# Performance work log

Hardware: AMD Instinct MI355X
Metric: run time of the kernel (lower is better)

## Reference

```python
import jax, jax.numpy as jnp
import numpy as np
from functools import partial

B, L, V = 64, 512, 20000
P, M = 150, 6          # total patterns, max pattern length
NEG = -1e9             # semiring zero (log-space)
END_STATES = np.repeat(np.array([3, 4, 5]), 50)  # pattern_len-1 per pattern


@jax.custom_vjp
def ste_heaviside(x):
    return (x > 0).astype(x.dtype)

def _ste_fwd(x):
    return ste_heaviside(x), None

def _ste_bwd(_, g):
    return (g,)  # straight-through identity (matches torch code path)

ste_heaviside.defvjp(_ste_fwd, _ste_bwd)


def setup_inputs() -> dict:
    key = jax.random.key(0)
    ks = jax.random.split(key, 8)
    return {
        "docs": jax.random.randint(ks[0], (B, L), 0, V),
        "doc_lens": jax.random.randint(ks[1], (B,), 1, L),
        "local_embeddings": jax.random.normal(ks[2], (300, V), jnp.float32),
        "diags": jax.random.normal(ks[3], (P * M, 300), jnp.float32) * 0.05,
        "bias": jax.random.normal(ks[4], (P * M, 1), jnp.float32) * 0.05,
        "wildcards": jax.random.normal(ks[5], (P, M - 1), jnp.float32) * 0.05,
        "ln_gamma": jnp.ones((P,), jnp.float32),
        "ln_beta": jnp.zeros((P,), jnp.float32),
        "linear_w": jax.random.normal(ks[6], (2, P), jnp.float32) * 0.05,
        "linear_b": jnp.zeros((2,), jnp.float32),
    }


def reference(docs, doc_lens, local_embeddings, diags, bias, wildcards,
              ln_gamma, ln_beta, linear_w, linear_b):
    end_states = jnp.asarray(END_STATES)                  # [P]
    pat_idx = jnp.arange(P)

    # transition matrices over local vocab, mapped into log-space semiring
    tm_vocab = jax.nn.log_sigmoid((diags @ local_embeddings + bias).T)  # [V, P*M]
    tm = tm_vocab[docs].reshape(B, L, P, M)               # [B,L,P,M]

    # wildcard transitions: semiring.times(one=0, log_sigmoid(wildcards))
    wild = jax.nn.log_sigmoid(wildcards)                  # [P, M-1]

    restart = jnp.zeros((B, P, 1), tm.dtype)              # semiring one
    hid0 = jnp.full((B, P, M), NEG, tm.dtype).at[:, :, 0].set(0.0)
    scores0 = jnp.full((B, P), NEG, tm.dtype)             # semiring zero

    def step(carry, inputs):
        hid, sc = carry
        t, tm_t = inputs                                  # tm_t: [B,P,M]
        main = jnp.concatenate([restart, hid[:, :, :-1] + tm_t[:, :, :-1]], axis=2)
        wildp = jnp.concatenate([restart, hid[:, :, :-1] + wild[None]], axis=2)
        hid = jnp.maximum(main, wildp)                    # semiring plus
        esv = hid[:, pat_idx, end_states]                 # [B,P]
        active = (doc_lens > t)[:, None]
        sc = jnp.where(active, jnp.maximum(sc, esv), sc)
        return (hid, sc), None

    xs = (jnp.arange(L), jnp.moveaxis(tm, 1, 0))          # [L], [L,B,P,M]
    (_, scores), _ = jax.lax.scan(step, (hid0, scores0), xs)

    scores = jnp.exp(scores)                              # from_semiring_to_outer
    mu = scores.mean(axis=-1, keepdims=True)
    var = scores.var(axis=-1, keepdims=True)
    norm = (scores - mu) * jax.lax.rsqrt(var + 1e-5) * ln_gamma + ln_beta
    binar = ste_heaviside(norm)
    return binar @ linear_w.T + linear_b
```

## Files before the change

kernel.cpp:

```cpp
#include <hip/hip_runtime.h>
#include <hip/hip_bf16.h>
#include <hip/hip_fp16.h>
#include <math.h>

#define B_   64
#define L_   512
#define V_   20000
#define P_   150
#define M_   6
#define KDIM 300
#define NOUT 750
#define CWS  752
#define NEGF (-1.0e9f)

#define BM 128
#define BN 128
#define BK 16
#define LDP 132

#define KP 320
#define NIT 10
#define NVG 157
#define NJ  6
#define TILE_U4 1024
#define SA 1024.0f
#define SB 16384.0f
#define INV24 (5.9604644775390625e-8f)

#define TCHUNK 32
#define NCHUNK (L_ / TCHUNK)
#define WARM   5
#define CS_STRIDE 160
#define KVBUF 3

typedef _Float16 f16x8 __attribute__((ext_vector_type(8)));
typedef float f32x16 __attribute__((ext_vector_type(16)));

__device__ __forceinline__ float logsigf(float x) {
    return fminf(x, 0.f) - log1pf(expf(-fabsf(x)));
}

__device__ __forceinline__ float logsigf_fast(float x) {
    return fminf(x, 0.f) - __logf(1.f + __expf(-fabsf(x)));
}

__device__ __forceinline__ void gload_lds16(const void* gp, void* lp) {
    __builtin_amdgcn_global_load_lds(
        (const __attribute__((address_space(1))) unsigned int*)gp,
        (__attribute__((address_space(3))) unsigned int*)lp, 16, 0, 0);
}


__global__ __launch_bounds__(256) void p12_split(
    const float* __restrict__ emb, const float* __restrict__ diags,
    uint4* __restrict__ a_t, uint4* __restrict__ b_t)
{
    __shared__ float T[64][132];
    const int t   = threadIdx.x;
    const int bid = blockIdx.x;

    if (bid < NVG * 5) {
        const int gx = bid % NVG;
        const int ky = bid / NVG;
        const int v0 = gx * 128;
        const int k0 = ky * 64;

        #pragma unroll
        for (int pass = 0; pass < 8; ++pass) {
            int flat = pass * 256 + t;
            int krow = flat >> 5;
            int c4   = (flat & 31) * 4;
            int kg   = k0 + krow;
            int v    = v0 + c4;
            float4 f = {0.f, 0.f, 0.f, 0.f};
            if (kg < KDIM && v + 3 < V_)
                f = *(const float4*)(emb + (size_t)kg * V_ + v);
            *(float4*)&T[krow][c4] = f;
        }
        __syncthreads();

        const int vv = t >> 1;
        const int kh = (t & 1) * 32;
        const int it = ky * 2 + (kh >> 5);
        const int v  = v0 + vv;
        if (v < V_) {
            union { ushort u[8]; uint4 q; } H[4], Lo[4];
            #pragma unroll
            for (int i = 0; i < 32; ++i) {
                float x = T[kh + i][vv] * SA;
                __half h = __float2half_rn(x);
                float rem = x - __half2float(h);
                H[i >> 3].u[i & 7]  = __half_as_ushort(h);
                Lo[i >> 3].u[i & 7] = __half_as_ushort(__float2half_rn(rem));
            }
            uint4* tile = a_t + ((size_t)gx * NIT + it) * TILE_U4;
            #pragma unroll
            for (int c = 0; c < 4; ++c) {
                tile[      c * 128 + vv] = H[c].q;
                tile[512 + c * 128 + vv] = Lo[c].q;
            }
        }
    } else {
        const int bidx = bid - NVG * 5;
        const int it   = bidx % NIT;
        const int j    = bidx / NIT;
        const int row  = t >> 1;
        const int qh   = (t & 1) * 2;
        const int n    = j * 128 + row;
        const bool nok = (n < NOUT);
        const int pm   = nok ? ((n / 5) * 6 + (n % 5)) : 0;
        uint4* tile = b_t + (size_t)bidx * TILE_U4;
        #pragma unroll
        for (int qq = 0; qq < 2; ++qq) {
            int q = qh + qq;
            union { ushort u[8]; uint4 v; } H, Lo;
            #pragma unroll
            for (int e = 0; e < 8; ++e) {
                int k = it * 32 + q * 8 + e;
                float x = (nok && k < KDIM) ? diags[(size_t)pm * KDIM + k] * SB : 0.f;
                __half h = __float2half_rn(x);
                float rem = x - __half2float(h);
                H.u[e]  = __half_as_ushort(h);
                Lo.u[e] = __half_as_ushort(__float2half_rn(rem));
            }
            tile[      q * 128 + row] = H.v;
            tile[512 + q * 128 + row] = Lo.v;
        }
    }
}

__global__ __launch_bounds__(256, 2) void k1m_gemm(
    const uint4* __restrict__ a_t, const uint4* __restrict__ b_t,
    const float* __restrict__ bias, const float* __restrict__ wildc,
    float* __restrict__ cw)
{
    const int bid  = blockIdx.x;
    const int xcd  = bid & 7;
    const int slot = bid >> 3;
    const int g    = xcd + 8 * (slot / 6);
    const int j    = slot % 6;
    if (g >= NVG) return;

    __shared__ uint4 sm[2][2048];
    const int t    = threadIdx.x;
    const int lane = t & 63;
    const int w    = t >> 6;
    const int wr   = w >> 1, wc = w & 1;
    const int v0   = g * 128;
    const int n0   = j * 128;

    const uint4* gsec = (w < 2)
        ? a_t + (size_t)g * NIT * TILE_U4 + w * 512
        : b_t + (size_t)j * NIT * TILE_U4 + (w - 2) * 512;

    const int fk16 = lane >> 5;
    const int fm   = lane & 31;

    f32x16 acc[2][2];
    #pragma unroll
    for (int i = 0; i < 2; ++i)
        #pragma unroll
        for (int jj = 0; jj < 2; ++jj)
            #pragma unroll
            for (int r = 0; r < 16; ++r) acc[i][jj][r] = 0.f;

    {
        const uint4* gp = gsec + lane;
        #pragma unroll
        for (int i = 0; i < 8; ++i)
            gload_lds16(gp + i * 64, &sm[0][w * 512 + i * 64 + lane]);
    }

    int cur = 0;
    for (int it = 0; it < NIT; ++it) {
        __syncthreads();

        if (it + 1 < NIT) {
            const uint4* gp = gsec + (size_t)(it + 1) * TILE_U4 + lane;
            #pragma unroll
            for (int i = 0; i < 8; ++i)
                gload_lds16(gp + i * 64, &sm[cur ^ 1][w * 512 + i * 64 + lane]);
        }

        const uint4* smc = sm[cur];
        #pragma unroll
        for (int s = 0; s < 2; ++s) {
            f16x8 A1[2], A2[2], B1[2], B2[2];
            const int q = s * 2 + fk16;
            #pragma unroll
            for (int ri = 0; ri < 2; ++ri) {
                A1[ri] = *(const f16x8*)&smc[(0 * 4 + q) * 128 + wr * 64 + ri * 32 + fm];
                A2[ri] = *(const f16x8*)&smc[(1 * 4 + q) * 128 + wr * 64 + ri * 32 + fm];
            }
            #pragma unroll
            for (int cj = 0; cj < 2; ++cj) {
                B1[cj] = *(const f16x8*)&smc[(2 * 4 + q) * 128 + wc * 64 + cj * 32 + fm];
                B2[cj] = *(const f16x8*)&smc[(3 * 4 + q) * 128 + wc * 64 + cj * 32 + fm];
            }
            #pragma unroll
            for (int ri = 0; ri < 2; ++ri)
                #pragma unroll
                for (int cj = 0; cj < 2; ++cj) {
                    acc[ri][cj] = __builtin_amdgcn_mfma_f32_32x32x16_f16(A1[ri], B1[cj], acc[ri][cj], 0, 0, 0);
                    acc[ri][cj] = __builtin_amdgcn_mfma_f32_32x32x16_f16(A1[ri], B2[cj], acc[ri][cj], 0, 0, 0);
                    acc[ri][cj] = __builtin_amdgcn_mfma_f32_32x32x16_f16(A2[ri], B1[cj], acc[ri][cj], 0, 0, 0);
                }
        }
        cur ^= 1;
    }

    float biasv[2], lwv[2]; int ncol[2]; bool nok[2];
    #pragma unroll
    for (int cj = 0; cj < 2; ++cj) {
        int n = n0 + wc * 64 + cj * 32 + fm;
        ncol[cj] = n;
        nok[cj]  = (n < NOUT);
        int nc = nok[cj] ? n : 0;
        int pm = (nc / 5) * 6 + (nc % 5);
        biasv[cj] = bias[pm];
        lwv[cj]   = logsigf_fast(wildc[nc]);
    }
    #pragma unroll
    for (int ri = 0; ri < 2; ++ri) {
        int vbase = v0 + wr * 64 + ri * 32 + 4 * fk16;
        #pragma unroll
        for (int cj = 0; cj < 2; ++cj) {
            if (!nok[cj]) continue;
            #pragma unroll
            for (int r = 0; r < 16; ++r) {
                int v = vbase + (r & 3) + 8 * (r >> 2);
                if (v < V_) {
                    float val = acc[ri][cj][r] * INV24 + biasv[cj];
                    __builtin_nontemporal_store(
                        fmaxf(logsigf_fast(val), lwv[cj]),
                        &cw[(size_t)v * CWS + ncol[cj]]);
                }
            }
        }
    }
}


__global__ __launch_bounds__(256) void k1_gemm_cw(
    const float* __restrict__ emb,
    const float* __restrict__ diags,
    const float* __restrict__ bias,
    const float* __restrict__ wildc,
    float* __restrict__ cw)
{
    __shared__ float As[BK][LDP];
    __shared__ float Bs[BK][LDP];

    const int tid = threadIdx.x;
    const int v0 = blockIdx.x * BM;
    const int n0 = blockIdx.y * BN;
    const int tx = tid & 15;
    const int ty = tid >> 4;

    float acc[8][8];
    #pragma unroll
    for (int i = 0; i < 8; ++i)
        #pragma unroll
        for (int j = 0; j < 8; ++j) acc[i][j] = 0.f;

    const int a_k = tid >> 4;
    const int a_v = (tid & 15) * 8;
    const int b_n   = tid >> 1;
    const int b_kof = (tid & 1) * 8;

    int  brow;
    bool bval;
    {
        int n = n0 + b_n;
        bval = (n < NOUT);
        brow = bval ? ((n / 5) * 6 + (n % 5)) : 0;
    }

    for (int k0 = 0; k0 < KDIM; k0 += BK) {
        {
            float4 f0 = {0,0,0,0}, f1 = {0,0,0,0};
            int k = k0 + a_k;
            if (k < KDIM) {
                const float* src = emb + (size_t)k * V_ + v0 + a_v;
                if (v0 + a_v + 3 < V_) f0 = *(const float4*)src;
                if (v0 + a_v + 7 < V_) f1 = *(const float4*)(src + 4);
            }
            *(float4*)&As[a_k][a_v]     = f0;
            *(float4*)&As[a_k][a_v + 4] = f1;
        }
        {
            float4 f = {0,0,0,0}, g = {0,0,0,0};
            if (bval) {
                const float* src = diags + (size_t)brow * KDIM + k0 + b_kof;
                if (k0 + b_kof + 3 < KDIM) f = *(const float4*)src;
                if (k0 + b_kof + 7 < KDIM) g = *(const float4*)(src + 4);
            }
            Bs[b_kof + 0][b_n] = f.x;
            Bs[b_kof + 1][b_n] = f.y;
            Bs[b_kof + 2][b_n] = f.z;
            Bs[b_kof + 3][b_n] = f.w;
            Bs[b_kof + 4][b_n] = g.x;
            Bs[b_kof + 5][b_n] = g.y;
            Bs[b_kof + 6][b_n] = g.z;
            Bs[b_kof + 7][b_n] = g.w;
        }
        __syncthreads();
        #pragma unroll
        for (int k = 0; k < BK; ++k) {
            float4 a0 = *(const float4*)&As[k][tx * 4];
            float4 a1 = *(const float4*)&As[k][64 + tx * 4];
            float4 b0 = *(const float4*)&Bs[k][ty * 8];
            float4 b1 = *(const float4*)&Bs[k][ty * 8 + 4];
            float av[8] = {a0.x, a0.y, a0.z, a0.w, a1.x, a1.y, a1.z, a1.w};
            float bv[8] = {b0.x, b0.y, b0.z, b0.w, b1.x, b1.y, b1.z, b1.w};
            #pragma unroll
            for (int i = 0; i < 8; ++i)
                #pragma unroll
                for (int j = 0; j < 8; ++j)
                    acc[i][j] = fmaf(av[i], bv[j], acc[i][j]);
        }
        __syncthreads();
    }

    float biasv[8], lwv[8];
    #pragma unroll
    for (int j = 0; j < 8; ++j) {
        int n  = n0 + ty * 8 + j;
        int nc = (n < NOUT) ? n : 0;
        int pm = (nc / 5) * 6 + (nc % 5);
        biasv[j] = bias[pm];
        lwv[j]   = logsigf(wildc[nc]);
    }
    #pragma unroll
    for (int i = 0; i < 8; ++i) {
        int v = v0 + ((i < 4) ? (tx * 4 + i) : (64 + tx * 4 + (i - 4)));
        if (v >= V_) continue;
        float r[8];
        #pragma unroll
        for (int j = 0; j < 8; ++j)
            r[j] = fmaxf(logsigf(acc[i][j] + biasv[j]), lwv[j]);
        float* dst = cw + (size_t)v * CWS + n0 + ty * 8;
        if (n0 + ty * 8     < NOUT) *(float4*)dst       = make_float4(r[0], r[1], r[2], r[3]);
        if (n0 + ty * 8 + 4 < NOUT) *(float4*)(dst + 4) = make_float4(r[4], r[5], r[6], r[7]);
    }
}


__global__ __launch_bounds__(192) void k2_scan(
    const int* __restrict__ docs,
    const int* __restrict__ doc_lens,
    const float* __restrict__ cw,
    float* __restrict__ cs)
{
    const int ci = blockIdx.x;
    const int b  = blockIdx.y;
    const int t0 = ci * TCHUNK;
    const int ts = (t0 >= WARM) ? (t0 - WARM) : 0;
    const int dl = doc_lens[b];
    const int te = min(t0 + TCHUNK, dl);
    const int nt = te - ts;

    __shared__ int   toks[TCHUNK + WARM];
    __shared__ float rows[KVBUF][3][768];

    const int t    = threadIdx.x;
    const int lane = t & 63;
    const int w    = t >> 6;

    if (t < TCHUNK + WARM) {
        int tt = ts + t;
        toks[t] = docs[b * L_ + min(tt, L_ - 1)];
    }
    __syncthreads();

    const int p      = t;
    const int e      = (p < 50) ? 3 : (p < 100) ? 4 : 5;
    const int warm_n = t0 - ts;
    float h1 = NEGF, h2 = NEGF, h3 = NEGF, h4 = NEGF, h5 = NEGF, sc = NEGF;

    const int nrounds = (nt > 0) ? (nt + 2) / 3 : 0;

    for (int r0 = 0; r0 < 2; ++r0) {
        if (r0 >= nrounds) break;
        int idx = min(3 * r0 + w, nt - 1);
        const char* rowp = (const char*)(cw + (size_t)toks[idx] * CWS);
        char* lbase = (char*)&rows[r0][w][0];
        #pragma unroll
        for (int jj = 0; jj < 3; ++jj)
            gload_lds16(rowp + jj * 1024 + lane * 16,
                        lbase + jj * 1024 + lane * 16);
    }

    int bufc = 0;
    for (int r = 0; r < nrounds; ++r) {
        if (r + 1 < nrounds) {
            asm volatile("s_waitcnt vmcnt(3)" ::: "memory");
        } else {
            asm volatile("s_waitcnt vmcnt(0)" ::: "memory");
        }
        __builtin_amdgcn_s_barrier();
        asm volatile("" ::: "memory");

        if (r + 2 < nrounds) {
            int rn  = r + 2;
            int idx = min(3 * rn + w, nt - 1);
            const char* rowp = (const char*)(cw + (size_t)toks[idx] * CWS);
            int bn = bufc + 2; if (bn >= KVBUF) bn -= KVBUF;
            char* lbase = (char*)&rows[bn][w][0];
            #pragma unroll
            for (int jj = 0; jj < 3; ++jj)
                gload_lds16(rowp + jj * 1024 + lane * 16,
                            lbase + jj * 1024 + lane * 16);
        }

        #pragma unroll
        for (int u = 0; u < 3; ++u) {
            int i2 = 3 * r + u;
            if (i2 >= nt) break;
            if (p < P_) {
                const float* rp = &rows[bufc][u][p * 5];
                float c0 = rp[0], c1 = rp[1], c2 = rp[2], c3 = rp[3], c4 = rp[4];
                h5 = h4 + c4;
                h4 = h3 + c3;
                h3 = h2 + c2;
                h2 = h1 + c1;
                h1 = c0;
                if (i2 >= warm_n) {
                    float esv = (e == 3) ? h3 : (e == 4) ? h4 : h5;
                    sc = fmaxf(sc, esv);
                }
            }
        }
        bufc = (bufc + 1 == KVBUF) ? 0 : bufc + 1;
    }
    if (p < P_) cs[(size_t)(b * NCHUNK + ci) * CS_STRIDE + p] = sc;
}

__device__ __forceinline__ float block_sum192(float v, volatile float* red, int tid) {
    #pragma unroll
    for (int off = 32; off > 0; off >>= 1) v += __shfl_down(v, off, 64);
    __syncthreads();
    if ((tid & 63) == 0) red[tid >> 6] = v;
    __syncthreads();
    return red[0] + red[1] + red[2];
}

__global__ __launch_bounds__(192) void k3_final(
    const float* __restrict__ cs,
    const float* __restrict__ gamma,
    const float* __restrict__ beta,
    const float* __restrict__ lw,
    const float* __restrict__ lb,
    float* __restrict__ out)
{
    __shared__ float red[3];
    const int b   = blockIdx.x;
    const int tid = threadIdx.x;
    float s = 0.f;
    if (tid < P_) {
        float m = NEGF;
        const float* row = cs + (size_t)b * NCHUNK * CS_STRIDE + tid;
        #pragma unroll
        for (int ci = 0; ci < NCHUNK; ++ci) m = fmaxf(m, row[ci * CS_STRIDE]);
        s = expf(m);
    }
    float mu = block_sum192(s, red, tid) * (1.f / P_);
    float d  = (tid < P_) ? (s - mu) : 0.f;
    float var = block_sum192(d * d, red, tid) * (1.f / P_);
    float bin = 0.f;
    if (tid < P_) {
        float norm = (s - mu) * rsqrtf(var + 1e-5f) * gamma[tid] + beta[tid];
        bin = (norm > 0.f) ? 1.f : 0.f;
    }
    float o0 = block_sum192((tid < P_) ? bin * lw[tid]      : 0.f, red, tid);
    float o1 = block_sum192((tid < P_) ? bin * lw[P_ + tid] : 0.f, red, tid);
    if (tid == 0) {
        out[b * 2 + 0] = o0 + lb[0];
        out[b * 2 + 1] = o1 + lb[1];
    }
}

extern "C" void kernel_launch(void* const* d_in, const int* in_sizes, int n_in,
                              void* d_out, int out_size, void* d_ws, size_t ws_size,
                              hipStream_t stream)
{
    const int*   docs  = (const int*)  d_in[0];
    const int*   dlens = (const int*)  d_in[1];
    const float* emb   = (const float*)d_in[2];
    const float* diags = (const float*)d_in[3];
    const float* bias  = (const float*)d_in[4];
    const float* wildc = (const float*)d_in[5];
    const float* gamma = (const float*)d_in[6];
    const float* beta  = (const float*)d_in[7];
    const float* lw    = (const float*)d_in[8];
    const float* lb    = (const float*)d_in[9];
    float* out = (float*)d_out;

    const size_t cw_b = (size_t)V_ * CWS * 4;
    const size_t cs_b = (size_t)B_ * NCHUNK * CS_STRIDE * 4;
    const size_t at_b = (size_t)NVG * NIT * TILE_U4 * 16;
    const size_t bt_b = (size_t)NJ  * NIT * TILE_U4 * 16;
    const size_t need = cw_b + cs_b + at_b + bt_b;

    char* base = (char*)d_ws;
    float* cw = (float*)base;
    float* cs = (float*)(base + cw_b);
    uint4* at = (uint4*)(base + cw_b + cs_b);
    uint4* bt = (uint4*)(base + cw_b + cs_b + at_b);

    if (ws_size >= need) {
        p12_split<<<NVG * 5 + NJ * NIT, 256, 0, stream>>>(emb, diags, at, bt);
        k1m_gemm<<<960, 256, 0, stream>>>(at, bt, bias, wildc, cw);
    } else {
        dim3 g1((V_ + BM - 1) / BM, (NOUT + BN - 1) / BN);
        k1_gemm_cw<<<g1, 256, 0, stream>>>(emb, diags, bias, wildc, cw);
    }

    dim3 g2(NCHUNK, B_);
    k2_scan<<<g2, 192, 0, stream>>>(docs, dlens, cw, cs);
    k3_final<<<B_, 192, 0, stream>>>(cs, gamma, beta, lw, lb, out);
}
```

Baseline: 155.5 us.

## Widen GEMM tile to 128x384 with 8 waves and register-staged prefetch

The fp16-split MFMA GEMM now gives each 512-thread block a 128x384 output tile (three B column tiles) instead of 128x128. Each A tile is loaded once per three B tiles, and the grid shrinks from 960 to 314 blocks. The async global-to-LDS loads are replaced by a two-deep register prefetch: global loads go into registers two iterations ahead and are written to double-buffered LDS after the compute. This costs more registers, more LDS (128KB per block) and fewer blocks, which may lower occupancy and parallelism. The XCD-aware block remapping is also dropped.

```diff
diff --git a/kernel.cpp b/kernel.cpp
--- a/kernel.cpp
+++ b/kernel.cpp
@@ -129,90 +129,119 @@
     }
 }
 
-__global__ __launch_bounds__(256, 2) void k1m_gemm(
+__global__ __launch_bounds__(512, 2) void k1m_gemm(
     const uint4* __restrict__ a_t, const uint4* __restrict__ b_t,
     const float* __restrict__ bias, const float* __restrict__ wildc,
     float* __restrict__ cw)
 {
-    const int bid  = blockIdx.x;
-    const int xcd  = bid & 7;
-    const int slot = bid >> 3;
-    const int g    = xcd + 8 * (slot / 6);
-    const int j    = slot % 6;
-    if (g >= NVG) return;
-
-    __shared__ uint4 sm[2][2048];
+    const int bid = blockIdx.x;
+    const int g   = bid >> 1;
+    const int h   = bid & 1;
+
+    __shared__ uint4 sm[2][4096];
     const int t    = threadIdx.x;
     const int lane = t & 63;
     const int w    = t >> 6;
-    const int wr   = w >> 1, wc = w & 1;
+    const int wr   = w >> 2;
+    const int wc   = w & 3;
     const int v0   = g * 128;
-    const int n0   = j * 128;
-
-    const uint4* gsec = (w < 2)
-        ? a_t + (size_t)g * NIT * TILE_U4 + w * 512
-        : b_t + (size_t)j * NIT * TILE_U4 + (w - 2) * 512;
 
     const int fk16 = lane >> 5;
     const int fm   = lane & 31;
 
-    f32x16 acc[2][2];
+    const uint4* abase = a_t + (size_t)g * NIT * TILE_U4;
+    const uint4* bbase[3];
+    #pragma unroll
+    for (int jj = 0; jj < 3; ++jj)
+        bbase[jj] = b_t + (size_t)(h * 3 + jj) * NIT * TILE_U4;
+
+    f32x16 acc[2][3];
     #pragma unroll
     for (int i = 0; i < 2; ++i)
         #pragma unroll
-        for (int jj = 0; jj < 2; ++jj)
+        for (int jj = 0; jj < 3; ++jj)
             #pragma unroll
             for (int r = 0; r < 16; ++r) acc[i][jj][r] = 0.f;
 
-    {
-        const uint4* gp = gsec + lane;
-        #pragma unroll
-        for (int i = 0; i < 8; ++i)
-            gload_lds16(gp + i * 64, &sm[0][w * 512 + i * 64 + lane]);
-    }
-
-    int cur = 0;
+    uint4 ra[8], rb[8];
+
+    #define LOAD_SET(R, IT)                                            \
+        do {                                                           \
+            const uint4* ab = abase + (size_t)(IT) * TILE_U4;          \
+            R[0] = ab[t];                                              \
+            R[1] = ab[512 + t];                                        \
+            _Pragma("unroll")                                          \
+            for (int jj = 0; jj < 3; ++jj) {                           \
+                const uint4* bb = bbase[jj] + (size_t)(IT) * TILE_U4;  \
+                R[2 + 2 * jj]     = bb[t];                             \
+                R[2 + 2 * jj + 1] = bb[512 + t];                       \
+            }                                                          \
+        } while (0)
+
+    #define WRITE_SET(R, BSEL)                                         \
+        do {                                                           \
+            uint4* smb = &sm[(BSEL)][0];                               \
+            smb[t]       = R[0];                                       \
+            smb[512 + t] = R[1];                                       \
+            _Pragma("unroll")                                          \
+            for (int jj = 0; jj < 3; ++jj) {                           \
+                smb[1024 + jj * 1024 + t]       = R[2 + 2 * jj];       \
+                smb[1024 + jj * 1024 + 512 + t] = R[2 + 2 * jj + 1];   \
+            }                                                          \
+        } while (0)
+
+    LOAD_SET(ra, 0);
+    WRITE_SET(ra, 0);
+    LOAD_SET(rb, 1);
+    __syncthreads();
+
+    #pragma unroll
     for (int it = 0; it < NIT; ++it) {
-        __syncthreads();
-
-        if (it + 1 < NIT) {
-            const uint4* gp = gsec + (size_t)(it + 1) * TILE_U4 + lane;
-            #pragma unroll
-            for (int i = 0; i < 8; ++i)
-                gload_lds16(gp + i * 64, &sm[cur ^ 1][w * 512 + i * 64 + lane]);
-        }
-
-        const uint4* smc = sm[cur];
+        if (it + 2 < NIT) {
+            if ((it & 1) == 0) { LOAD_SET(ra, it + 2); }
+            else               { LOAD_SET(rb, it + 2); }
+        }
+
+        const uint4* smc = &sm[it & 1][0];
         #pragma unroll
         for (int s = 0; s < 2; ++s) {
-            f16x8 A1[2], A2[2], B1[2], B2[2];
             const int q = s * 2 + fk16;
+            f16x8 A1[2], A2[2], B1[3], B2[3];
             #pragma unroll
             for (int ri = 0; ri < 2; ++ri) {
-                A1[ri] = *(const f16x8*)&smc[(0 * 4 + q) * 128 + wr * 64 + ri * 32 + fm];
-                A2[ri] = *(const f16x8*)&smc[(1 * 4 + q) * 128 + wr * 64 + ri * 32 + fm];
-            }
-            #pragma unroll
-            for (int cj = 0; cj < 2; ++cj) {
-                B1[cj] = *(const f16x8*)&smc[(2 * 4 + q) * 128 + wc * 64 + cj * 32 + fm];
-                B2[cj] = *(const f16x8*)&smc[(3 * 4 + q) * 128 + wc * 64 + cj * 32 + fm];
+                A1[ri] = *(const f16x8*)&smc[      q * 128 + wr * 64 + ri * 32 + fm];
+                A2[ri] = *(const f16x8*)&smc[512 + q * 128 + wr * 64 + ri * 32 + fm];
+            }
+            #pragma unroll
+            for (int cj = 0; cj < 3; ++cj) {
+                const int nc  = wc * 96 + cj * 32;
+                const int bofs = 1024 + (nc >> 7) * 1024 + q * 128 + (nc & 127) + fm;
+                B1[cj] = *(const f16x8*)&smc[bofs];
+                B2[cj] = *(const f16x8*)&smc[bofs + 512];
             }
             #pragma unroll
             for (int ri = 0; ri < 2; ++ri)
                 #pragma unroll
-                for (int cj = 0; cj < 2; ++cj) {
+                for (int cj = 0; cj < 3; ++cj) {
                     acc[ri][cj] = __builtin_amdgcn_mfma_f32_32x32x16_f16(A1[ri], B1[cj], acc[ri][cj], 0, 0, 0);
                     acc[ri][cj] = __builtin_amdgcn_mfma_f32_32x32x16_f16(A1[ri], B2[cj], acc[ri][cj], 0, 0, 0);
                     acc[ri][cj] = __builtin_amdgcn_mfma_f32_32x32x16_f16(A2[ri], B1[cj], acc[ri][cj], 0, 0, 0);
                 }
         }
-        cur ^= 1;
-    }
-
-    float biasv[2], lwv[2]; int ncol[2]; bool nok[2];
-    #pragma unroll
-    for (int cj = 0; cj < 2; ++cj) {
-        int n = n0 + wc * 64 + cj * 32 + fm;
+
+        if (it + 1 < NIT) {
+            if ((it & 1) == 0) { WRITE_SET(rb, (it + 1) & 1); }
+            else               { WRITE_SET(ra, (it + 1) & 1); }
+            __syncthreads();
+        }
+    }
+    #undef LOAD_SET
+    #undef WRITE_SET
+
+    float biasv[3], lwv[3]; int ncol[3]; bool nok[3];
+    #pragma unroll
+    for (int cj = 0; cj < 3; ++cj) {
+        int n = h * 384 + wc * 96 + cj * 32 + fm;
         ncol[cj] = n;
         nok[cj]  = (n < NOUT);
         int nc = nok[cj] ? n : 0;
@@ -224,7 +253,7 @@
     for (int ri = 0; ri < 2; ++ri) {
         int vbase = v0 + wr * 64 + ri * 32 + 4 * fk16;
         #pragma unroll
-        for (int cj = 0; cj < 2; ++cj) {
+        for (int cj = 0; cj < 3; ++cj) {
             if (!nok[cj]) continue;
             #pragma unroll
             for (int r = 0; r < 16; ++r) {
@@ -510,7 +539,7 @@
 
     if (ws_size >= need) {
         p12_split<<<NVG * 5 + NJ * NIT, 256, 0, stream>>>(emb, diags, at, bt);
-        k1m_gemm<<<960, 256, 0, stream>>>(at, bt, bias, wildc, cw);
+        k1m_gemm<<<NVG * 2, 512, 0, stream>>>(at, bt, bias, wildc, cw);
     } else {
         dim3 g1((V_ + BM - 1) / BM, (NOUT + BN - 1) / BN);
         k1_gemm_cw<<<g1, 256, 0, stream>>>(emb, diags, bias, wildc, cw);
```

Result: slower. 234.9 us (+51.1%).

## Enlarge GEMM tiles to 256x256 with register-staged double buffering

Applied to the files above, without the earlier changes.

The vocab-by-pattern GEMM now uses 512-thread blocks computing 256x256 output tiles (240 blocks instead of 960 blocks of 128x128). Global-to-LDS loads go through registers with a two-iteration prefetch, replacing the direct global-to-LDS loads. The aim is more operand reuse per LDS byte and fewer blocks. Nontemporal stores become plain stores. In exchange the kernel needs more registers (8 accumulators per wave) and 128KB of LDS per block, and a grid of 240 blocks may leave CUs on the 256-CU part underused. The epilogue-heavy output write may still dominate.

```diff
diff --git a/kernel.cpp b/kernel.cpp
--- a/kernel.cpp
+++ b/kernel.cpp
@@ -129,76 +129,100 @@
     }
 }
 
-__global__ __launch_bounds__(256, 2) void k1m_gemm(
+__global__ __launch_bounds__(512) void k1m_gemm(
     const uint4* __restrict__ a_t, const uint4* __restrict__ b_t,
     const float* __restrict__ bias, const float* __restrict__ wildc,
     float* __restrict__ cw)
 {
-    const int bid  = blockIdx.x;
-    const int xcd  = bid & 7;
-    const int slot = bid >> 3;
-    const int g    = xcd + 8 * (slot / 6);
-    const int j    = slot % 6;
-    if (g >= NVG) return;
-
-    __shared__ uint4 sm[2][2048];
+    const int bid = blockIdx.x;
+    const int c   = bid / 24;
+    const int r   = bid % 24;
+    const int gp  = c * 8 + (r & 7);
+    const int h   = r >> 3;
+    if (gp >= 79) return;
+
+    __shared__ uint4 sm[2][4096];
     const int t    = threadIdx.x;
     const int lane = t & 63;
     const int w    = t >> 6;
-    const int wr   = w >> 1, wc = w & 1;
-    const int v0   = g * 128;
-    const int n0   = j * 128;
-
-    const uint4* gsec = (w < 2)
-        ? a_t + (size_t)g * NIT * TILE_U4 + w * 512
-        : b_t + (size_t)j * NIT * TILE_U4 + (w - 2) * 512;
-
+    const int wr   = w >> 2;
+    const int wc   = w & 3;
     const int fk16 = lane >> 5;
     const int fm   = lane & 31;
 
-    f32x16 acc[2][2];
-    #pragma unroll
-    for (int i = 0; i < 2; ++i)
+    const int ga = 2 * gp;
+    const int gb = (2 * gp + 1 < NVG) ? (2 * gp + 1) : (NVG - 1);
+    const uint4* abase0 = a_t + (size_t)ga * NIT * TILE_U4;
+    const uint4* abase1 = a_t + (size_t)gb * NIT * TILE_U4;
+    const uint4* bbase0 = b_t + (size_t)(2 * h)     * NIT * TILE_U4;
+    const uint4* bbase1 = b_t + (size_t)(2 * h + 1) * NIT * TILE_U4;
+
+    f32x16 acc[4][2];
+    #pragma unroll
+    for (int i = 0; i < 4; ++i)
         #pragma unroll
         for (int jj = 0; jj < 2; ++jj)
             #pragma unroll
-            for (int r = 0; r < 16; ++r) acc[i][jj][r] = 0.f;
-
-    {
-        const uint4* gp = gsec + lane;
-        #pragma unroll
-        for (int i = 0; i < 8; ++i)
-            gload_lds16(gp + i * 64, &sm[0][w * 512 + i * 64 + lane]);
-    }
-
-    int cur = 0;
+            for (int e = 0; e < 16; ++e) acc[i][jj][e] = 0.f;
+
+    uint4 rg[8];
+
+    #define LOAD_SET(IT)                                   \
+        do {                                               \
+            const size_t o = (size_t)(IT) * TILE_U4;       \
+            rg[0] = abase0[o + t];                         \
+            rg[1] = abase0[o + 512 + t];                   \
+            rg[2] = abase1[o + t];                         \
+            rg[3] = abase1[o + 512 + t];                   \
+            rg[4] = bbase0[o + t];                         \
+            rg[5] = bbase0[o + 512 + t];                   \
+            rg[6] = bbase1[o + t];                         \
+            rg[7] = bbase1[o + 512 + t];                   \
+        } while (0)
+
+    #define WRITE_SET(BSEL)                                \
+        do {                                               \
+            uint4* smb = &sm[(BSEL)][0];                   \
+            smb[        t] = rg[0];                        \
+            smb[ 512 +  t] = rg[1];                        \
+            smb[1024 +  t] = rg[2];                        \
+            smb[1536 +  t] = rg[3];                        \
+            smb[2048 +  t] = rg[4];                        \
+            smb[2560 +  t] = rg[5];                        \
+            smb[3072 +  t] = rg[6];                        \
+            smb[3584 +  t] = rg[7];                        \
+        } while (0)
+
+    LOAD_SET(0);
+    WRITE_SET(0);
+    LOAD_SET(1);
+    __syncthreads();
+
+    #pragma unroll
     for (int it = 0; it < NIT; ++it) {
-        __syncthreads();
-
-        if (it + 1 < NIT) {
-            const uint4* gp = gsec + (size_t)(it + 1) * TILE_U4 + lane;
-            #pragma unroll
-            for (int i = 0; i < 8; ++i)
-                gload_lds16(gp + i * 64, &sm[cur ^ 1][w * 512 + i * 64 + lane]);
-        }
-
-        const uint4* smc = sm[cur];
+        if (it + 1 < NIT) WRITE_SET((it + 1) & 1);
+        if (it + 2 < NIT) LOAD_SET(it + 2);
+
+        const uint4* smc = &sm[it & 1][0];
         #pragma unroll
         for (int s = 0; s < 2; ++s) {
-            f16x8 A1[2], A2[2], B1[2], B2[2];
             const int q = s * 2 + fk16;
-            #pragma unroll
-            for (int ri = 0; ri < 2; ++ri) {
-                A1[ri] = *(const f16x8*)&smc[(0 * 4 + q) * 128 + wr * 64 + ri * 32 + fm];
-                A2[ri] = *(const f16x8*)&smc[(1 * 4 + q) * 128 + wr * 64 + ri * 32 + fm];
+            f16x8 A1[4], A2[4], B1[2], B2[2];
+            #pragma unroll
+            for (int ri = 0; ri < 4; ++ri) {
+                const int ao = wr * 1024 + q * 128 + ri * 32 + fm;
+                A1[ri] = *(const f16x8*)&smc[ao];
+                A2[ri] = *(const f16x8*)&smc[ao + 512];
             }
             #pragma unroll
             for (int cj = 0; cj < 2; ++cj) {
-                B1[cj] = *(const f16x8*)&smc[(2 * 4 + q) * 128 + wc * 64 + cj * 32 + fm];
-                B2[cj] = *(const f16x8*)&smc[(3 * 4 + q) * 128 + wc * 64 + cj * 32 + fm];
-            }
-            #pragma unroll
-            for (int ri = 0; ri < 2; ++ri)
+                const int colb = wc * 64 + cj * 32;
+                const int bo = 2048 + (colb >> 7) * 1024 + q * 128 + (colb & 127) + fm;
+                B1[cj] = *(const f16x8*)&smc[bo];
+                B2[cj] = *(const f16x8*)&smc[bo + 512];
+            }
+            #pragma unroll
+            for (int ri = 0; ri < 4; ++ri)
                 #pragma unroll
                 for (int cj = 0; cj < 2; ++cj) {
                     acc[ri][cj] = __builtin_amdgcn_mfma_f32_32x32x16_f16(A1[ri], B1[cj], acc[ri][cj], 0, 0, 0);
@@ -206,13 +230,16 @@
                     acc[ri][cj] = __builtin_amdgcn_mfma_f32_32x32x16_f16(A2[ri], B1[cj], acc[ri][cj], 0, 0, 0);
                 }
         }
-        cur ^= 1;
-    }
+
+        if (it + 1 < NIT) __syncthreads();
+    }
+    #undef LOAD_SET
+    #undef WRITE_SET
 
     float biasv[2], lwv[2]; int ncol[2]; bool nok[2];
     #pragma unroll
     for (int cj = 0; cj < 2; ++cj) {
-        int n = n0 + wc * 64 + cj * 32 + fm;
+        int n = h * 256 + wc * 64 + cj * 32 + fm;
         ncol[cj] = n;
         nok[cj]  = (n < NOUT);
         int nc = nok[cj] ? n : 0;
@@ -220,20 +247,19 @@
         biasv[cj] = bias[pm];
         lwv[cj]   = logsigf_fast(wildc[nc]);
     }
-    #pragma unroll
-    for (int ri = 0; ri < 2; ++ri) {
-        int vbase = v0 + wr * 64 + ri * 32 + 4 * fk16;
+    const int v0 = gp * 256;
+    #pragma unroll
+    for (int ri = 0; ri < 4; ++ri) {
+        int vbase = v0 + wr * 128 + ri * 32 + 4 * fk16;
         #pragma unroll
         for (int cj = 0; cj < 2; ++cj) {
             if (!nok[cj]) continue;
             #pragma unroll
-            for (int r = 0; r < 16; ++r) {
-                int v = vbase + (r & 3) + 8 * (r >> 2);
+            for (int e = 0; e < 16; ++e) {
+                int v = vbase + (e & 3) + 8 * (e >> 2);
                 if (v < V_) {
-                    float val = acc[ri][cj][r] * INV24 + biasv[cj];
-                    __builtin_nontemporal_store(
-                        fmaxf(logsigf_fast(val), lwv[cj]),
-                        &cw[(size_t)v * CWS + ncol[cj]]);
+                    float val = acc[ri][cj][e] * INV24 + biasv[cj];
+                    cw[(size_t)v * CWS + ncol[cj]] = fmaxf(logsigf_fast(val), lwv[cj]);
                 }
             }
         }
@@ -510,7 +536,7 @@
 
     if (ws_size >= need) {
         p12_split<<<NVG * 5 + NJ * NIT, 256, 0, stream>>>(emb, diags, at, bt);
-        k1m_gemm<<<960, 256, 0, stream>>>(at, bt, bias, wildc, cw);
+        k1m_gemm<<<240, 512, 0, stream>>>(at, bt, bias, wildc, cw);
     } else {
         dim3 g1((V_ + BM - 1) / BM, (NOUT + BN - 1) / BN);
         k1_gemm_cw<<<g1, 256, 0, stream>>>(emb, diags, bias, wildc, cw);
```

New measurement: 178.6 us. 1.15x slower.
